# Performance work log

Hardware: AMD Instinct MI355X
Metric: run time of the kernel (lower is better)

The kernel has to match this reference:

```python
import jax, jax.numpy as jnp
import numpy as np

KDIM = 128
NHEADS = 8
CAUSAL = True


def setup_inputs() -> dict:
    key = jax.random.key(0)
    ks = jax.random.split(key, 9)
    t, b = 1024, 8
    hk = KDIM * NHEADS
    s = 1.0 / np.sqrt(KDIM)
    return {
        "x":  jax.random.normal(ks[0], (t, b, KDIM), dtype=jnp.float32),
        "Wk": jax.random.uniform(ks[1], (hk, KDIM), jnp.float32, -s, s),
        "bk": jax.random.uniform(ks[2], (hk,), jnp.float32, -s, s),
        "Wq": jax.random.uniform(ks[3], (hk, KDIM), jnp.float32, -s, s),
        "bq": jax.random.uniform(ks[4], (hk,), jnp.float32, -s, s),
        "Wv": jax.random.uniform(ks[5], (hk, KDIM), jnp.float32, -s, s),
        "bv": jax.random.uniform(ks[6], (hk,), jnp.float32, -s, s),
        "Wo": jax.random.uniform(ks[7], (KDIM, hk), jnp.float32, -1.0/np.sqrt(hk), 1.0/np.sqrt(hk)),
        "bo": jax.random.uniform(ks[8], (KDIM,), jnp.float32, -1.0/np.sqrt(hk), 1.0/np.sqrt(hk)),
    }


def reference(x, Wk, bk, Wq, bq, Wv, bv, Wo, bo):
    t, b, _ = x.shape
    h, d = NHEADS, KDIM
    xb = jnp.transpose(x, (1, 0, 2))  # (b, t, d)

    def proj(W, bias):
        # (b, t, h*d) -> (b, h, t, d)
        y = xb @ W.T + bias
        return jnp.transpose(y.reshape(b, t, h, d), (0, 2, 1, 3))

    k_ = proj(Wk, bk)
    q_ = proj(Wq, bq)
    v_ = proj(Wv, bv)

    # NOTE: original computes bmm(key, query^T): rows indexed by KEY position.
    raw = jnp.einsum("bhik,bhjk->bhij", k_, q_) / jnp.sqrt(jnp.float32(d))
    if CAUSAL:
        # mask entries with col > row (upper triangle, offset 1)
        iidx = jnp.arange(t)[:, None]
        jidx = jnp.arange(t)[None, :]
        raw = jnp.where(jidx > iidx, -jnp.inf, raw)
    # softmax over the QUERY axis (dim=2 of the (bh,t,t) view == last axis here)
    att = jax.nn.softmax(raw, axis=-1)
    out = jnp.einsum("bhij,bhjd->bhid", att, v_)  # (b, h, t, d)
    out = jnp.transpose(out, (2, 0, 1, 3)).reshape(t, b, h * d)
    return out @ Wo.T + bo
```

## Files before the change

kernel.cpp:

```cpp
#include <hip/hip_runtime.h>
#include <hip/hip_bf16.h>

typedef __bf16 bf16_t;
typedef __bf16 bf16x2_t __attribute__((ext_vector_type(2)));
typedef __bf16 bf16x4_t __attribute__((ext_vector_type(4)));
typedef __bf16 bf16x8 __attribute__((ext_vector_type(8)));
typedef float f32x4 __attribute__((ext_vector_type(4)));
typedef float f32x16 __attribute__((ext_vector_type(16)));
typedef unsigned int u32x2 __attribute__((ext_vector_type(2)));

#define T_SEQ 1024
#define BATCH 8
#define NH 8
#define DH 128
#define HKDIM 1024

static __device__ __forceinline__ f32x4 mfma16(bf16x8 a, bf16x8 b, f32x4 c) {
    return __builtin_amdgcn_mfma_f32_16x16x32_bf16(a, b, c, 0, 0, 0);
}
static __device__ __forceinline__ f32x16 mfma32(bf16x8 a, bf16x8 b, f32x16 c) {
    return __builtin_amdgcn_mfma_f32_32x32x16_bf16(a, b, c, 0, 0, 0);
}

static __device__ __forceinline__ unsigned pk2(float a, float b) {
    bf16x2_t t;
    t[0] = (bf16_t)a;
    t[1] = (bf16_t)b;
    union { bf16x2_t v; unsigned u; } c;
    c.v = t;
    return c.u;
}

static __device__ __forceinline__ void plswap(unsigned& a, unsigned& b) {
    u32x2 r = __builtin_amdgcn_permlane32_swap(a, b, false, false);
    a = r[0];
    b = r[1];
}

static __device__ __forceinline__ float swap_partner(float x) {
    u32x2 r = __builtin_amdgcn_permlane32_swap(__float_as_uint(x),
                                               __float_as_uint(x), false, false);
    return __uint_as_float((threadIdx.x & 32) ? r[0] : r[1]);
}

__global__ __launch_bounds__(256) void convert_kernel(
        const float* __restrict__ x,
        const float* __restrict__ Wk, const float* __restrict__ Wq,
        const float* __restrict__ Wv, const float* __restrict__ Wo,
        bf16_t* __restrict__ xb, bf16_t* __restrict__ w3,
        bf16_t* __restrict__ wo) {
    const int n1 = T_SEQ * BATCH * DH;
    const int n2 = n1 + 3 * HKDIM * DH;
    const int n3 = n2 + DH * HKDIM;
    const int i = (blockIdx.x * 256 + threadIdx.x) * 4;
    if (i >= n3) return;
    const float* src;
    bf16_t* dst;
    if (i < n1) {
        int d = i & 127, t = (i >> 7) & 1023, b = i >> 17;
        src = x + (t * BATCH + b) * DH + d;
        dst = xb + i;
    } else if (i < n2) {
        int j = i - n1;
        int p = j >> 17;
        const float* W = (p == 0) ? Wk : (p == 1 ? Wq : Wv);
        src = W + (j & 131071);
        dst = w3 + j;
    } else {
        int j = i - n2;
        src = Wo + j;
        dst = wo + j;
    }
    f32x4 v = *(const f32x4*)src;
    bf16x4_t o;
    o[0] = (bf16_t)v[0]; o[1] = (bf16_t)v[1];
    o[2] = (bf16_t)v[2]; o[3] = (bf16_t)v[3];
    *(bf16x4_t*)dst = o;
}

__global__ __launch_bounds__(256) void proj_kernel(
        const bf16_t* __restrict__ xb, const bf16_t* __restrict__ w3,
        const float* __restrict__ bk, const float* __restrict__ bq,
        const float* __restrict__ bv,
        bf16_t* __restrict__ kbuf, bf16_t* __restrict__ qbuf,
        bf16_t* __restrict__ vtbuf) {
    const int lane = threadIdx.x & 63;
    const int wave = threadIdx.x >> 6;
    const int lr = lane & 15, lq = lane >> 4;
    const int rm_base = blockIdx.x * 128;
    const int p = blockIdx.y >> 3;
    const int h = blockIdx.y & 7;
    const int cb0 = p * 1024 + h * 128;
    const int cw0 = h * 128;
    const bool isV = (p == 2);

    __shared__ bf16_t sL[128][136];

    bf16x8 aF[2][4];
#pragma unroll
    for (int rg = 0; rg < 2; ++rg) {
        const int row = rm_base + rg * 64 + wave * 16 + lr;
#pragma unroll
        for (int kc = 0; kc < 4; ++kc)
            aF[rg][kc] = *(const bf16x8*)(xb + (size_t)row * DH + kc * 32 + lq * 8);
    }

    const bf16_t* wbase = w3 + (size_t)(cb0 + lr) * DH + lq * 8;
    bf16x8 kcur[4], knxt[4];
#pragma unroll
    for (int kc = 0; kc < 4; ++kc)
        kcur[kc] = *(const bf16x8*)(wbase + kc * 32);

    const float* bias_kq = (p == 0) ? bk : bq;
    bf16_t* dst = (p == 0) ? kbuf : qbuf;

#pragma unroll
    for (int nc = 0; nc < 8; ++nc) {
        if (nc < 7) {
            const bf16_t* wn = wbase + (size_t)(nc + 1) * 16 * DH;
#pragma unroll
            for (int kc = 0; kc < 4; ++kc)
                knxt[kc] = *(const bf16x8*)(wn + kc * 32);
        }

        f32x4 acc[2] = {{0.f, 0.f, 0.f, 0.f}, {0.f, 0.f, 0.f, 0.f}};
        if (!isV) {
#pragma unroll
            for (int rg = 0; rg < 2; ++rg)
#pragma unroll
                for (int kc = 0; kc < 4; ++kc)
                    acc[rg] = mfma16(kcur[kc], aF[rg][kc], acc[rg]);

            const f32x4 b4 = *(const f32x4*)(bias_kq + cw0 + nc * 16 + lq * 4);
#pragma unroll
            for (int rg = 0; rg < 2; ++rg) {
                bf16x4_t o4;
#pragma unroll
                for (int r = 0; r < 4; ++r)
                    o4[r] = (bf16_t)(acc[rg][r] + b4[r]);
                *(bf16x4_t*)&sL[rg * 64 + wave * 16 + lr][nc * 16 + lq * 4] = o4;
            }
        } else {
#pragma unroll
            for (int rg = 0; rg < 2; ++rg)
#pragma unroll
                for (int kc = 0; kc < 4; ++kc)
                    acc[rg] = mfma16(aF[rg][kc], kcur[kc], acc[rg]);

            const float bias = bv[cw0 + nc * 16 + lr];
#pragma unroll
            for (int rg = 0; rg < 2; ++rg)
#pragma unroll
                for (int r = 0; r < 4; ++r)
                    sL[nc * 16 + lr][rg * 64 + wave * 16 + lq * 4 + r] =
                        (bf16_t)(acc[rg][r] + bias);
        }
        if (nc < 7) {
#pragma unroll
            for (int kc = 0; kc < 4; ++kc) kcur[kc] = knxt[kc];
        }
    }

    __syncthreads();
    const int tid = threadIdx.x;
    if (!isV) {
        const int tr = tid >> 4;
        const int ck = tid & 15;
#pragma unroll
        for (int ps = 0; ps < 8; ++ps) {
            const int t_local = ps * 16 + tr;
            const int row = rm_base + t_local;
            const int bb = row >> 10, tt = row & 1023;
            bf16x8 v = *(const bf16x8*)&sL[t_local][ck * 8];
            *(bf16x8*)(dst + ((size_t)(bb * NH + h) * T_SEQ + tt) * DH + ck * 8) = v;
        }
    } else {
        const int dr = tid >> 4;
        const int ck = tid & 15;
        const int bb = blockIdx.x >> 3;
        const int t0 = (blockIdx.x & 7) * 128;
#pragma unroll
        for (int ps = 0; ps < 8; ++ps) {
            const int d = ps * 16 + dr;
            bf16x8 v = *(const bf16x8*)&sL[d][ck * 8];
            *(bf16x8*)(vtbuf + ((size_t)(bb * NH + h) * DH + d) * T_SEQ +
                       t0 + ck * 8) = v;
        }
    }
}

__global__ __launch_bounds__(256, 2) void attn_kernel(
        const bf16_t* __restrict__ kbuf, const bf16_t* __restrict__ qbuf,
        const bf16_t* __restrict__ vtb, bf16_t* __restrict__ obuf) {
    const int bx = blockIdx.x;
    const int T = (bx < 256) ? (7 - (bx >> 6)) : ((bx - 256) >> 6);
    const int bh = bx & 63;
    const int b = bh >> 3, h = bh & 7;
    const int wv = threadIdx.x >> 6;
    const int lane = threadIdx.x & 63;
    const int li = lane & 31;
    const int hi = lane >> 5;
    const int i0 = T * 128 + wv * 32;
    const int cmax = 4 * T + wv;
    const int nrounds = 2 * T + 2;

    const bf16_t* Qp = kbuf + (size_t)bh * T_SEQ * DH;
    const bf16_t* Kp = qbuf + (size_t)bh * T_SEQ * DH;
    const bf16_t* Vt = vtb + (size_t)bh * DH * T_SEQ;

    __shared__ bf16_t kL[64][136];
    __shared__ bf16_t vL[128][72];

    bf16x8 qf[8];
#pragma unroll
    for (int s = 0; s < 8; ++s)
        qf[s] = *(const bf16x8*)(Qp + (size_t)(i0 + li) * DH + s * 16 + hi * 8);

    f32x16 oacc[4];
#pragma unroll
    for (int c = 0; c < 4; ++c)
#pragma unroll
        for (int e = 0; e < 16; ++e) oacc[c][e] = 0.f;

    float m = 0.f, l = 0.f;
    const float C = 0.08838834764831845f * 1.4426950408889634f;

    const int tid = threadIdx.x;
    const int krow = tid >> 2;
    const int kcol = (tid & 3) * 32;
    const int vrow = tid >> 1;
    const int vcol = (tid & 1) * 32;
    const bf16_t* kgsrc = Kp + (size_t)krow * DH + kcol;
    const bf16_t* vgsrc = Vt + (size_t)vrow * T_SEQ + vcol;

    bf16x8 kr[4], vr[4];
#pragma unroll
    for (int i = 0; i < 4; ++i) {
        kr[i] = *(const bf16x8*)(kgsrc + i * 8);
        vr[i] = *(const bf16x8*)(vgsrc + i * 8);
    }

    for (int rd = 0; rd < nrounds; ++rd) {
        __syncthreads();
#pragma unroll
        for (int i = 0; i < 4; ++i) {
            *(bf16x8*)&kL[krow][kcol + i * 8] = kr[i];
            *(bf16x8*)&vL[vrow][vcol + i * 8] = vr[i];
        }
        if (rd + 1 < nrounds) {
            const bf16_t* kn = kgsrc + (size_t)(rd + 1) * 64 * DH;
            const bf16_t* vn = vgsrc + (size_t)(rd + 1) * 64;
#pragma unroll
            for (int i = 0; i < 4; ++i) {
                kr[i] = *(const bf16x8*)(kn + i * 8);
                vr[i] = *(const bf16x8*)(vn + i * 8);
            }
        }
        __syncthreads();

#pragma unroll
        for (int jj = 0; jj < 2; ++jj) {
            const int c32 = rd * 2 + jj;
            if (c32 > cmax) continue;

            bf16x8 ka[8];
#pragma unroll
            for (int s = 0; s < 8; ++s)
                ka[s] = *(const bf16x8*)&kL[jj * 32 + li][s * 16 + hi * 8];

            f32x16 sc;
#pragma unroll
            for (int e = 0; e < 16; ++e) sc[e] = 0.f;
            __builtin_amdgcn_s_setprio(1);
#pragma unroll
            for (int s = 0; s < 8; ++s) sc = mfma32(ka[s], qf[s], sc);
            __builtin_amdgcn_s_setprio(0);

            f32x16 sv;
#pragma unroll
            for (int e = 0; e < 16; ++e) sv[e] = sc[e] * C;
            if (c32 == cmax) {
#pragma unroll
                for (int r = 0; r < 16; ++r) {
                    const int jrow = (r & 3) + 8 * (r >> 2) + 4 * hi;
                    if (jrow > li) sv[r] = -1e30f;
                }
            }

            float pm = sv[0];
#pragma unroll
            for (int r = 1; r < 16; ++r) pm = fmaxf(pm, sv[r]);
            pm = fmaxf(pm, swap_partner(pm));

            if (!__all(pm <= m + 8.f)) {
                const float mn = fmaxf(m, pm);
                const float f = exp2f(m - mn);
                m = mn;
                l *= f;
#pragma unroll
                for (int cc = 0; cc < 4; ++cc)
#pragma unroll
                    for (int e = 0; e < 16; ++e) oacc[cc][e] *= f;
            }

            float ls = 0.f;
            unsigned Wp[8];
#pragma unroll
            for (int q = 0; q < 4; ++q) {
                const float p0 = exp2f(sv[4 * q + 0] - m);
                const float p1 = exp2f(sv[4 * q + 1] - m);
                const float p2 = exp2f(sv[4 * q + 2] - m);
                const float p3 = exp2f(sv[4 * q + 3] - m);
                ls += (p0 + p1) + (p2 + p3);
                Wp[2 * q] = pk2(p0, p1);
                Wp[2 * q + 1] = pk2(p2, p3);
            }
            l += ls;

            plswap(Wp[0], Wp[2]);
            plswap(Wp[1], Wp[3]);
            plswap(Wp[4], Wp[6]);
            plswap(Wp[5], Wp[7]);
            union { unsigned u[4]; bf16x8 v; } pb0, pb1;
            pb0.u[0] = Wp[0]; pb0.u[1] = Wp[1]; pb0.u[2] = Wp[2]; pb0.u[3] = Wp[3];
            pb1.u[0] = Wp[4]; pb1.u[1] = Wp[5]; pb1.u[2] = Wp[6]; pb1.u[3] = Wp[7];

            bf16x8 va[8];
#pragma unroll
            for (int n = 0; n < 4; ++n) {
                va[2 * n]     = *(const bf16x8*)&vL[li + 32 * n][jj * 32 + hi * 8];
                va[2 * n + 1] = *(const bf16x8*)&vL[li + 32 * n][jj * 32 + hi * 8 + 16];
            }
            __builtin_amdgcn_s_setprio(1);
            oacc[0] = mfma32(va[0], pb0.v, oacc[0]);
            oacc[0] = mfma32(va[1], pb1.v, oacc[0]);
            oacc[1] = mfma32(va[2], pb0.v, oacc[1]);
            oacc[1] = mfma32(va[3], pb1.v, oacc[1]);
            oacc[2] = mfma32(va[4], pb0.v, oacc[2]);
            oacc[2] = mfma32(va[5], pb1.v, oacc[2]);
            oacc[3] = mfma32(va[6], pb0.v, oacc[3]);
            oacc[3] = mfma32(va[7], pb1.v, oacc[3]);
            __builtin_amdgcn_s_setprio(0);
        }
    }

    const float lfull = l + swap_partner(l);
    const float inv = 1.f / lfull;
    __syncthreads();
    bf16_t (*oL)[136] = (bf16_t(*)[136])kL;
    bf16_t* base = (wv < 2) ? &kL[0][0] : &vL[0][0];
    const int rloc = (wv & 1) * 32 + li;
#pragma unroll
    for (int c = 0; c < 4; ++c)
#pragma unroll
        for (int q = 0; q < 4; ++q) {
            bf16x4_t o4;
#pragma unroll
            for (int rr = 0; rr < 4; ++rr)
                o4[rr] = (bf16_t)(oacc[c][4 * q + rr] * inv);
            *(bf16x4_t*)(base + (size_t)rloc * 136 + c * 32 + q * 8 + 4 * hi) = o4;
        }
    __syncthreads();
    {
        const int tr = tid >> 4;
        const int ck = tid & 15;
#pragma unroll
        for (int ps = 0; ps < 8; ++ps) {
            const int rl = ps * 16 + tr;
            const bf16_t* src = ((rl & 64) ? &vL[0][0] : &kL[0][0]) +
                                (size_t)(rl & 63) * 136 + ck * 8;
            bf16x8 v = *(const bf16x8*)src;
            const int row = T * 128 + rl;
            *(bf16x8*)(obuf + ((size_t)b * T_SEQ + row) * HKDIM + h * DH + ck * 8) = v;
        }
    }
}

__global__ __launch_bounds__(256) void outproj_kernel(
        const bf16_t* __restrict__ obuf, const bf16_t* __restrict__ wo,
        const float* __restrict__ bo, float* __restrict__ out) {
    const int lane = threadIdx.x & 63, wave = threadIdx.x >> 6;
    const int lr = lane & 15, lq = lane >> 4;
    const int rm0 = blockIdx.x * 16;
    __shared__ float red[4][8][256];

    f32x4 acc[8];
#pragma unroll
    for (int g = 0; g < 8; ++g) acc[g] = {0.f, 0.f, 0.f, 0.f};
#pragma unroll 2
    for (int k8 = 0; k8 < 8; ++k8) {
        const int kc = wave * 8 + k8;
        bf16x8 aF = *(const bf16x8*)(obuf + (size_t)(rm0 + lr) * HKDIM + kc * 32 + lq * 8);
#pragma unroll
        for (int g = 0; g < 8; ++g) {
            bf16x8 bF = *(const bf16x8*)(wo + (size_t)(g * 16 + lr) * HKDIM + kc * 32 + lq * 8);
            acc[g] = mfma16(aF, bF, acc[g]);
        }
    }
#pragma unroll
    for (int g = 0; g < 8; ++g)
        *(f32x4*)&red[wave][g][lane * 4] = acc[g];
    __syncthreads();
#pragma unroll
    for (int gi = 0; gi < 2; ++gi) {
        const int g = wave * 2 + gi;
        f32x4 s = *(const f32x4*)&red[0][g][lane * 4];
#pragma unroll
        for (int w = 1; w < 4; ++w) {
            f32x4 t = *(const f32x4*)&red[w][g][lane * 4];
            s[0] += t[0]; s[1] += t[1]; s[2] += t[2]; s[3] += t[3];
        }
        const int col = g * 16 + lr;
        const float bias = bo[col];
#pragma unroll
        for (int r = 0; r < 4; ++r) {
            const int row = rm0 + lq * 4 + r;
            const int bb = row >> 10, tt = row & 1023;
            out[((size_t)tt * BATCH + bb) * DH + col] = s[r] + bias;
        }
    }
}

extern "C" void kernel_launch(void* const* d_in, const int* in_sizes, int n_in,
                              void* d_out, int out_size, void* d_ws, size_t ws_size,
                              hipStream_t stream) {
    const float* x  = (const float*)d_in[0];
    const float* Wk = (const float*)d_in[1];
    const float* bk = (const float*)d_in[2];
    const float* Wq = (const float*)d_in[3];
    const float* bq = (const float*)d_in[4];
    const float* Wv = (const float*)d_in[5];
    const float* bv = (const float*)d_in[6];
    const float* Wo = (const float*)d_in[7];
    const float* bo = (const float*)d_in[8];
    float* out = (float*)d_out;

    char* ws = (char*)d_ws;
    size_t off = 0;
    bf16_t* xb  = (bf16_t*)(ws + off); off += (size_t)BATCH * T_SEQ * DH * 2;
    bf16_t* w3  = (bf16_t*)(ws + off); off += (size_t)3 * HKDIM * DH * 2;
    bf16_t* wo  = (bf16_t*)(ws + off); off += (size_t)DH * HKDIM * 2;
    bf16_t* kb  = (bf16_t*)(ws + off); off += (size_t)BATCH * NH * T_SEQ * DH * 2;
    bf16_t* qb  = (bf16_t*)(ws + off); off += (size_t)BATCH * NH * T_SEQ * DH * 2;
    bf16_t* vtb = (bf16_t*)(ws + off); off += (size_t)BATCH * NH * T_SEQ * DH * 2;
    bf16_t* ob  = (bf16_t*)(ws + off); off += (size_t)BATCH * T_SEQ * HKDIM * 2;

    convert_kernel<<<1536, 256, 0, stream>>>(x, Wk, Wq, Wv, Wo, xb, w3, wo);
    proj_kernel<<<dim3(64, 24), 256, 0, stream>>>(xb, w3, bk, bq, bv, kb, qb, vtb);
    attn_kernel<<<512, 256, 0, stream>>>(kb, qb, vtb, ob);
    outproj_kernel<<<512, 256, 0, stream>>>(ob, wo, bo, out);
}
```

Measured before the change: 100.2 us.

## Double-buffer K/V LDS tiles in attention and preload A operands in outproj

The attention kernel now keeps two LDS buffers for K and V tiles. The next tile is stored to the alternate buffer after compute, which leaves one barrier per round instead of two. The output staging now uses the flattened double-sized kL buffer. The outproj kernel preloads all eight A fragments up front and fully unrolls the k loop so more loads are in flight. The cost is twice the LDS for the attention block, which may lower occupancy, and higher register pressure in outproj.

```diff
diff --git a/kernel.cpp b/kernel.cpp
--- a/kernel.cpp
+++ b/kernel.cpp
@@ -208,8 +208,8 @@
     const bf16_t* Kp = qbuf + (size_t)bh * T_SEQ * DH;
     const bf16_t* Vt = vtb + (size_t)bh * DH * T_SEQ;
 
-    __shared__ bf16_t kL[64][136];
-    __shared__ bf16_t vL[128][72];
+    __shared__ bf16_t kL[2][64][136];
+    __shared__ bf16_t vL[2][128][72];
 
     bf16x8 qf[8];
 #pragma unroll
@@ -239,24 +239,20 @@
         kr[i] = *(const bf16x8*)(kgsrc + i * 8);
         vr[i] = *(const bf16x8*)(vgsrc + i * 8);
     }
+#pragma unroll
+    for (int i = 0; i < 4; ++i) {
+        *(bf16x8*)&kL[0][krow][kcol + i * 8] = kr[i];
+        *(bf16x8*)&vL[0][vrow][vcol + i * 8] = vr[i];
+    }
+#pragma unroll
+    for (int i = 0; i < 4; ++i) {
+        kr[i] = *(const bf16x8*)(kgsrc + (size_t)64 * DH + i * 8);
+        vr[i] = *(const bf16x8*)(vgsrc + 64 + i * 8);
+    }
+    __syncthreads();
 
     for (int rd = 0; rd < nrounds; ++rd) {
-        __syncthreads();
-#pragma unroll
-        for (int i = 0; i < 4; ++i) {
-            *(bf16x8*)&kL[krow][kcol + i * 8] = kr[i];
-            *(bf16x8*)&vL[vrow][vcol + i * 8] = vr[i];
-        }
-        if (rd + 1 < nrounds) {
-            const bf16_t* kn = kgsrc + (size_t)(rd + 1) * 64 * DH;
-            const bf16_t* vn = vgsrc + (size_t)(rd + 1) * 64;
-#pragma unroll
-            for (int i = 0; i < 4; ++i) {
-                kr[i] = *(const bf16x8*)(kn + i * 8);
-                vr[i] = *(const bf16x8*)(vn + i * 8);
-            }
-        }
-        __syncthreads();
+        const int cur = rd & 1;
 
 #pragma unroll
         for (int jj = 0; jj < 2; ++jj) {
@@ -266,7 +262,7 @@
             bf16x8 ka[8];
 #pragma unroll
             for (int s = 0; s < 8; ++s)
-                ka[s] = *(const bf16x8*)&kL[jj * 32 + li][s * 16 + hi * 8];
+                ka[s] = *(const bf16x8*)&kL[cur][jj * 32 + li][s * 16 + hi * 8];
 
             f32x16 sc;
 #pragma unroll
@@ -328,8 +324,8 @@
             bf16x8 va[8];
 #pragma unroll
             for (int n = 0; n < 4; ++n) {
-                va[2 * n]     = *(const bf16x8*)&vL[li + 32 * n][jj * 32 + hi * 8];
-                va[2 * n + 1] = *(const bf16x8*)&vL[li + 32 * n][jj * 32 + hi * 8 + 16];
+                va[2 * n]     = *(const bf16x8*)&vL[cur][li + 32 * n][jj * 32 + hi * 8];
+                va[2 * n + 1] = *(const bf16x8*)&vL[cur][li + 32 * n][jj * 32 + hi * 8 + 16];
             }
             __builtin_amdgcn_s_setprio(1);
             oacc[0] = mfma32(va[0], pb0.v, oacc[0]);
@@ -342,14 +338,31 @@
             oacc[3] = mfma32(va[7], pb1.v, oacc[3]);
             __builtin_amdgcn_s_setprio(0);
         }
+
+        if (rd + 1 < nrounds) {
+            const int nxt = cur ^ 1;
+#pragma unroll
+            for (int i = 0; i < 4; ++i) {
+                *(bf16x8*)&kL[nxt][krow][kcol + i * 8] = kr[i];
+                *(bf16x8*)&vL[nxt][vrow][vcol + i * 8] = vr[i];
+            }
+            if (rd + 2 < nrounds) {
+                const bf16_t* kn = kgsrc + (size_t)(rd + 2) * 64 * DH;
+                const bf16_t* vn = vgsrc + (size_t)(rd + 2) * 64;
+#pragma unroll
+                for (int i = 0; i < 4; ++i) {
+                    kr[i] = *(const bf16x8*)(kn + i * 8);
+                    vr[i] = *(const bf16x8*)(vn + i * 8);
+                }
+            }
+        }
+        __syncthreads();
     }
 
     const float lfull = l + swap_partner(l);
     const float inv = 1.f / lfull;
-    __syncthreads();
-    bf16_t (*oL)[136] = (bf16_t(*)[136])kL;
-    bf16_t* base = (wv < 2) ? &kL[0][0] : &vL[0][0];
-    const int rloc = (wv & 1) * 32 + li;
+    bf16_t* oflat = &kL[0][0][0];
+    const int rl = wv * 32 + li;
 #pragma unroll
     for (int c = 0; c < 4; ++c)
 #pragma unroll
@@ -358,7 +371,7 @@
 #pragma unroll
             for (int rr = 0; rr < 4; ++rr)
                 o4[rr] = (bf16_t)(oacc[c][4 * q + rr] * inv);
-            *(bf16x4_t*)(base + (size_t)rloc * 136 + c * 32 + q * 8 + 4 * hi) = o4;
+            *(bf16x4_t*)(oflat + (size_t)rl * 136 + c * 32 + q * 8 + 4 * hi) = o4;
         }
     __syncthreads();
     {
@@ -366,11 +379,9 @@
         const int ck = tid & 15;
 #pragma unroll
         for (int ps = 0; ps < 8; ++ps) {
-            const int rl = ps * 16 + tr;
-            const bf16_t* src = ((rl & 64) ? &vL[0][0] : &kL[0][0]) +
-                                (size_t)(rl & 63) * 136 + ck * 8;
-            bf16x8 v = *(const bf16x8*)src;
-            const int row = T * 128 + rl;
+            const int rlr = ps * 16 + tr;
+            bf16x8 v = *(const bf16x8*)(oflat + (size_t)rlr * 136 + ck * 8);
+            const int row = T * 128 + rlr;
             *(bf16x8*)(obuf + ((size_t)b * T_SEQ + row) * HKDIM + h * DH + ck * 8) = v;
         }
     }
@@ -384,17 +395,22 @@
     const int rm0 = blockIdx.x * 16;
     __shared__ float red[4][8][256];
 
+    const bf16_t* abase = obuf + (size_t)(rm0 + lr) * HKDIM + wave * 256 + lq * 8;
+    bf16x8 aA[8];
+#pragma unroll
+    for (int k8 = 0; k8 < 8; ++k8)
+        aA[k8] = *(const bf16x8*)(abase + k8 * 32);
+
     f32x4 acc[8];
 #pragma unroll
     for (int g = 0; g < 8; ++g) acc[g] = {0.f, 0.f, 0.f, 0.f};
-#pragma unroll 2
+#pragma unroll
     for (int k8 = 0; k8 < 8; ++k8) {
         const int kc = wave * 8 + k8;
-        bf16x8 aF = *(const bf16x8*)(obuf + (size_t)(rm0 + lr) * HKDIM + kc * 32 + lq * 8);
 #pragma unroll
         for (int g = 0; g < 8; ++g) {
             bf16x8 bF = *(const bf16x8*)(wo + (size_t)(g * 16 + lr) * HKDIM + kc * 32 + lq * 8);
-            acc[g] = mfma16(aF, bF, acc[g]);
+            acc[g] = mfma16(aA[k8], bF, acc[g]);
         }
     }
 #pragma unroll
```

Measured after the change: 94.74 us (median of 2 runs). 1.06x faster.
